# Kernel optimization log

Measured on AMD Instinct MI355X. Metric: run time of the kernel, lower is better.

Reference implementation:

```python
import jax, jax.numpy as jnp
import numpy as np
import math

B, S, N_UNITS, D_K = 8, 2048, 1024, 512


def setup_inputs() -> dict:
    key = jax.random.key(0)
    ks = jax.random.split(key, 8)
    scale = 1.0 / math.sqrt(N_UNITS)
    query = jax.random.normal(ks[0], (B, S, N_UNITS), dtype=jnp.float32)
    k_in = jax.random.normal(ks[1], (B, S, N_UNITS), dtype=jnp.float32)
    v_in = jax.random.normal(ks[2], (B, S, N_UNITS), dtype=jnp.float32)
    # custom multiplicative mask: causal lower-triangular, broadcast over batch
    mask = jnp.broadcast_to(jnp.tril(jnp.ones((S, S), dtype=jnp.float32)), (B, S, S))
    Wq = jax.random.normal(ks[3], (N_UNITS, D_K), dtype=jnp.float32) * scale
    Wk = jax.random.normal(ks[4], (N_UNITS, D_K), dtype=jnp.float32) * scale
    Wv = jax.random.normal(ks[5], (N_UNITS, D_K), dtype=jnp.float32) * scale
    bq = jnp.zeros((D_K,), dtype=jnp.float32)
    bk = jnp.zeros((D_K,), dtype=jnp.float32)
    bv = jnp.zeros((D_K,), dtype=jnp.float32)
    return {"query": query, "key": k_in, "value": v_in, "mask": mask,
            "Wq": Wq, "bq": bq, "Wk": Wk, "bk": bk, "Wv": Wv, "bv": bv}


def reference(query, key, value, mask, Wq, bq, Wk, bk, Wv, bv):
    d_k = Wq.shape[-1]
    Q = jnp.einsum('bsn,nd->bsd', query, Wq) + bq  # [B,S,Dk]
    K = jnp.einsum('bsn,nd->bsd', key, Wk) + bk
    V = jnp.einsum('bsn,nd->bsd', value, Wv) + bv
    # scores [B,S,S]
    x_hat = jnp.einsum('bqd,bkd->bqk', Q, K) / jnp.sqrt(jnp.float32(d_k))
    # custom multiplicative mask: x*mask - 1e9*(1-mask)
    x_hat_masked = x_hat * mask - 1e9 * (1.0 - mask)
    attn = jax.nn.softmax(x_hat_masked, axis=-1)
    # dropout = 0.0 (eval mode) -> identity
    out = jnp.einsum('bqk,bkd->bqd', attn, V)
    return out
```

## Files before the change

kernel.cpp:

```cpp
#include <hip/hip_runtime.h>

typedef __bf16 bf16_t;
typedef __attribute__((ext_vector_type(4))) __bf16 bf16x4;
typedef __attribute__((ext_vector_type(8))) __bf16 bf16x8;
typedef __attribute__((ext_vector_type(4))) float f32x4;

#define B_    8
#define S_    2048
#define NU    1024
#define DK    512
#define MROWS (B_ * S_)
#define PBATCH (128 * 128 * 136)

#define WAITVM(N) asm volatile("s_waitcnt vmcnt(" #N ")" ::: "memory")
#define WAITLG    asm volatile("s_waitcnt lgkmcnt(0)" ::: "memory")
#define BAR       __builtin_amdgcn_s_barrier()

__device__ __forceinline__ f32x4 mfma16(bf16x8 a, bf16x8 b, f32x4 c) {
  return __builtin_amdgcn_mfma_f32_16x16x32_bf16(a, b, c, 0, 0, 0);
}

__device__ __forceinline__ void async_load16(const void* g, void* l) {
  __builtin_amdgcn_global_load_lds(
      (const __attribute__((address_space(1))) unsigned int*)g,
      (__attribute__((address_space(3))) unsigned int*)l, 16, 0, 0);
}

__global__ __launch_bounds__(256) void transpose_w_kernel(
    const float* __restrict__ Wq, const float* __restrict__ Wk,
    const float* __restrict__ Wv, bf16_t* __restrict__ Wt) {
  const float* W = (blockIdx.z == 0) ? Wq : (blockIdx.z == 1) ? Wk : Wv;
  bf16_t* Wo = Wt + (size_t)blockIdx.z * DK * NU;
  __shared__ float tile[32][33];
  const int t = threadIdx.x;
  const int r = t >> 5, c = t & 31;
  const int kbase = blockIdx.y * 32, nbase = blockIdx.x * 32;
#pragma unroll
  for (int i = 0; i < 4; ++i)
    tile[r + i * 8][c] = W[(size_t)(kbase + r + i * 8) * DK + nbase + c];
  __syncthreads();
#pragma unroll
  for (int i = 0; i < 4; ++i)
    Wo[(size_t)(nbase + r + i * 8) * NU + kbase + c] = (bf16_t)tile[c][r + i * 8];
}

__global__ __launch_bounds__(256) void qkv_gemm_kernel(
    const float* __restrict__ q_in, const float* __restrict__ k_in,
    const float* __restrict__ v_in, const bf16_t* __restrict__ Wt,
    const float* __restrict__ bq, const float* __restrict__ bk,
    const float* __restrict__ bv, bf16_t* __restrict__ Qo,
    bf16_t* __restrict__ Ko, bf16_t* __restrict__ Vt) {
  const int z = blockIdx.y;
  const float* X = (z == 0) ? q_in : (z == 1) ? k_in : v_in;
  const bf16_t* Wz = Wt + (size_t)z * DK * NU;
  const float* bias = (z == 0) ? bq : (z == 1) ? bk : bv;

  __shared__ __align__(16) unsigned char smem[81920];
  float* A0 = (float*)smem;
  bf16_t* B0 = (bf16_t*)(smem + 8192);
  float* A1 = (float*)(smem + 40960);
  bf16_t* B1 = (bf16_t*)(smem + 49152);

  const int tid = threadIdx.x;
  const int wave = tid >> 6, lane = tid & 63;
  const int l16 = lane & 15, quad = lane >> 4;
  const int m0 = blockIdx.x * 64;
  const int ar = tid >> 3, ac = tid & 7;
  const int asrc = (ac ^ (ar & 7)) << 2;
  const int br = tid >> 2, bc = tid & 3;
  const int bsrc = (bc ^ (br & 3)) << 3;
  const int sw = l16 & 7;

  f32x4 acc[4][8] = {};

#define QKV_STAGE(An, Bn, K0)                                                 \
  { _Pragma("unroll") for (int j = 0; j < 2; ++j)                             \
      async_load16(X + (size_t)(m0 + j * 32 + ar) * NU + (K0) + asrc,         \
                   &(An)[(j * 32 + ar) * 32 + (ac << 2)]);                    \
    _Pragma("unroll") for (int j = 0; j < 8; ++j)                             \
      async_load16(Wz + (size_t)(j * 64 + br) * NU + (K0) + bsrc,             \
                   &(Bn)[(j * 64 + br) * 32 + (bc << 3)]); }

#define QKV_COMPUTE(Ac, Bc)                                                   \
  { bf16x8 af[4], bfr[8];                                                     \
    _Pragma("unroll") for (int i = 0; i < 4; ++i) {                           \
      const int row = i * 16 + l16;                                           \
      const f32x4 x0 = *(const f32x4*)&(Ac)[row * 32 + ((quad * 2) ^ sw) * 4];\
      const f32x4 x1 =                                                        \
          *(const f32x4*)&(Ac)[row * 32 + (((quad * 2) | 1) ^ sw) * 4];       \
      bf16x8 t;                                                               \
      _Pragma("unroll") for (int j = 0; j < 4; ++j) {                         \
        t[j] = (bf16_t)x0[j]; t[j + 4] = (bf16_t)x1[j]; }                     \
      af[i] = t; }                                                            \
    _Pragma("unroll") for (int j = 0; j < 8; ++j) {                           \
      const int row = wave * 128 + j * 16 + l16;                              \
      bfr[j] = *(const bf16x8*)&(Bc)[row * 32 + ((quad ^ (l16 & 3)) << 3)]; } \
    _Pragma("unroll") for (int i = 0; i < 4; ++i)                             \
      _Pragma("unroll") for (int j = 0; j < 8; ++j)                           \
        acc[i][j] = mfma16(af[i], bfr[j], acc[i][j]); }

  QKV_STAGE(A0, B0, 0)
  for (int ks = 0; ks < 32; ks += 2) {
    QKV_STAGE(A1, B1, (ks + 1) * 32)
    WAITVM(10); BAR;
    QKV_COMPUTE(A0, B0)
    WAITLG; BAR;
    if (ks + 2 < 32) { QKV_STAGE(A0, B0, (ks + 2) * 32) WAITVM(10); }
    else { WAITVM(0); }
    BAR;
    QKV_COMPUTE(A1, B1)
    WAITLG; BAR;
  }

  if (z != 2) {
    bf16_t* Out = (z == 0) ? Qo : Ko;
#pragma unroll
    for (int j = 0; j < 8; ++j) {
      const int cn = wave * 128 + j * 16 + l16;
      const float bz = bias[cn];
#pragma unroll
      for (int i = 0; i < 4; ++i) {
        const int rm = m0 + i * 16 + quad * 4;
#pragma unroll
        for (int r = 0; r < 4; ++r)
          Out[(size_t)(rm + r) * DK + cn] = (bf16_t)(acc[i][j][r] + bz);
      }
    }
  } else {
    bf16_t* Ts = (bf16_t*)smem;
#pragma unroll
    for (int j = 0; j < 8; ++j) {
      const int cn = wave * 128 + j * 16 + l16;
      const float bz = bias[cn];
#pragma unroll
      for (int i = 0; i < 4; ++i) {
        const int rs = i * 16 + quad * 4;
        bf16x4 t;
#pragma unroll
        for (int r = 0; r < 4; ++r) t[r] = (bf16_t)(acc[i][j][r] + bz);
        *(bf16x4*)&Ts[cn * 68 + rs] = t;
      }
    }
    WAITLG; BAR;
    const int bb = m0 >> 11, s0 = m0 & 2047;
#pragma unroll
    for (int rr = 0; rr < 2; ++rr) {
      const int row = rr * 256 + tid;
      bf16_t* dst = Vt + ((size_t)bb * DK + row) * S_ + s0;
      const bf16_t* src = &Ts[row * 68];
#pragma unroll
      for (int k = 0; k < 8; ++k)
        *(bf16x8*)(dst + k * 8) = *(const bf16x8*)(src + k * 8);
    }
  }
#undef QKV_STAGE
#undef QKV_COMPUTE
}

__global__ __launch_bounds__(256) void zerol_kernel(float* __restrict__ L) {
  ((f32x4*)L)[blockIdx.x * 256 + threadIdx.x] = f32x4{0.f, 0.f, 0.f, 0.f};
}

__global__ __launch_bounds__(256) void qk_p_kernel(
    const bf16_t* __restrict__ Q, const bf16_t* __restrict__ K,
    bf16_t* __restrict__ P, float* __restrict__ L) {
  const int bx = blockIdx.x;
  const int b = bx & 7;
  const int t = bx >> 3;
  int mt = 0;
  while (((mt + 1) * (mt + 2)) / 2 <= t) ++mt;
  const int nt = t - (mt * (mt + 1)) / 2;
  const int klen = (mt + 1) * 128;

  __shared__ __align__(16) bf16_t As[2][128 * 32];
  __shared__ __align__(16) bf16_t Bs[2][128 * 32];

  const int tid = threadIdx.x;
  const int wave = tid >> 6, lane = tid & 63;
  const int l16 = lane & 15, quad = lane >> 4;
  const int wm = (wave >> 1) * 64, wn = (wave & 1) * 64;
  const int br = tid >> 2, bc = tid & 3;
  const int bsrc = (bc ^ ((br >> 1) & 3)) << 3;
  const int sw2 = (l16 >> 1) & 3;

  const bf16_t* Ag = Q + (size_t)(b * S_ + mt * 128) * DK;
  const bf16_t* Bg = K + (size_t)(b * S_ + nt * 128) * DK;

  f32x4 acc[4][4] = {};

#define P1_STAGE(BUF, K0)                                                     \
  { _Pragma("unroll") for (int j = 0; j < 2; ++j)                             \
      async_load16(Ag + (size_t)(j * 64 + br) * DK + (K0) + bsrc,             \
                   &As[BUF][(j * 64 + br) * 32 + (bc << 3)]);                 \
    _Pragma("unroll") for (int j = 0; j < 2; ++j)                             \
      async_load16(Bg + (size_t)(j * 64 + br) * DK + (K0) + bsrc,             \
                   &Bs[BUF][(j * 64 + br) * 32 + (bc << 3)]); }

#define P1_COMPUTE(BUF)                                                       \
  { bf16x8 af[4], bfr[4];                                                     \
    _Pragma("unroll") for (int i = 0; i < 4; ++i)                             \
      af[i] = *(const bf16x8*)                                                \
          &As[BUF][(wm + i * 16 + l16) * 32 + ((quad ^ sw2) << 3)];           \
    _Pragma("unroll") for (int j = 0; j < 4; ++j)                             \
      bfr[j] = *(const bf16x8*)                                               \
          &Bs[BUF][(wn + j * 16 + l16) * 32 + ((quad ^ sw2) << 3)];           \
    _Pragma("unroll") for (int i = 0; i < 4; ++i)                             \
      _Pragma("unroll") for (int j = 0; j < 4; ++j)                           \
        acc[i][j] = mfma16(af[i], bfr[j], acc[i][j]); }

  P1_STAGE(0, 0)
  for (int ks = 0; ks < 16; ks += 2) {
    P1_STAGE(1, (ks + 1) * 32)
    WAITVM(4); BAR;
    P1_COMPUTE(0)
    WAITLG; BAR;
    if (ks + 2 < 16) { P1_STAGE(0, (ks + 2) * 32) WAITVM(4); }
    else { WAITVM(0); }
    BAR;
    P1_COMPUTE(1)
    WAITLG; BAR;
  }

  const float scale = 0.04419417382415922f;
  bf16_t* Pt = P + (size_t)b * PBATCH + (size_t)8192 * mt * (mt + 1);
  float* Lb = L + b * S_ + mt * 128;
#pragma unroll
  for (int i = 0; i < 4; ++i) {
#pragma unroll
    for (int r = 0; r < 4; ++r) {
      const int lrow = wm + i * 16 + quad * 4 + r;
      const int srow = mt * 128 + lrow;
      float rsum = 0.f;
#pragma unroll
      for (int j = 0; j < 4; ++j) {
        const int scol = nt * 128 + wn + j * 16 + l16;
        const float p =
            (scol > srow) ? 0.f : __expf(acc[i][j][r] * scale - 10.0f);
        rsum += p;
        Pt[(size_t)lrow * klen + scol] = (bf16_t)p;
      }
#pragma unroll
      for (int off = 8; off >= 1; off >>= 1)
        rsum += __shfl_xor(rsum, off, 64);
      if (l16 == 0) atomicAdd(&Lb[lrow], rsum);
    }
  }
#undef P1_STAGE
#undef P1_COMPUTE
}

__global__ __launch_bounds__(256) void pv_kernel(
    const bf16_t* __restrict__ P, const bf16_t* __restrict__ Vt,
    const float* __restrict__ L, float* __restrict__ Out) {
  const int bx = blockIdx.x;
  const int b = bx & 7;
  const int u = bx >> 3;
  const int mt = 15 - (u >> 2);
  const int d0 = (u & 3) * 128;
  const int klen = (mt + 1) * 128;
  const int NS = (mt + 1) * 4;

  __shared__ __align__(16) bf16_t As[2][128 * 32];
  __shared__ __align__(16) bf16_t Bs[2][128 * 32];

  const int tid = threadIdx.x;
  const int wave = tid >> 6, lane = tid & 63;
  const int l16 = lane & 15, quad = lane >> 4;
  const int wm = (wave >> 1) * 64, wn = (wave & 1) * 64;
  const int br = tid >> 2, bc = tid & 3;
  const int bsrc = (bc ^ ((br >> 1) & 3)) << 3;
  const int sw2 = (l16 >> 1) & 3;

  const bf16_t* Ag = P + (size_t)b * PBATCH + (size_t)8192 * mt * (mt + 1);
  const bf16_t* Bg = Vt + ((size_t)b * DK + d0) * S_;

  f32x4 acc[4][4] = {};

#define P2_STAGE(BUF, K0)                                                     \
  { _Pragma("unroll") for (int j = 0; j < 2; ++j)                             \
      async_load16(Ag + (size_t)(j * 64 + br) * klen + (K0) + bsrc,           \
                   &As[BUF][(j * 64 + br) * 32 + (bc << 3)]);                 \
    _Pragma("unroll") for (int j = 0; j < 2; ++j)                             \
      async_load16(Bg + (size_t)(j * 64 + br) * S_ + (K0) + bsrc,             \
                   &Bs[BUF][(j * 64 + br) * 32 + (bc << 3)]); }

#define P2_COMPUTE(BUF)                                                       \
  { bf16x8 af[4], bfr[4];                                                     \
    _Pragma("unroll") for (int i = 0; i < 4; ++i)                             \
      af[i] = *(const bf16x8*)                                                \
          &As[BUF][(wm + i * 16 + l16) * 32 + ((quad ^ sw2) << 3)];           \
    _Pragma("unroll") for (int j = 0; j < 4; ++j)                             \
      bfr[j] = *(const bf16x8*)                                               \
          &Bs[BUF][(wn + j * 16 + l16) * 32 + ((quad ^ sw2) << 3)];           \
    _Pragma("unroll") for (int i = 0; i < 4; ++i)                             \
      _Pragma("unroll") for (int j = 0; j < 4; ++j)                           \
        acc[i][j] = mfma16(af[i], bfr[j], acc[i][j]); }

  P2_STAGE(0, 0)
  for (int ks = 0; ks < NS; ks += 2) {
    P2_STAGE(1, (ks + 1) * 32)
    WAITVM(4); BAR;
    P2_COMPUTE(0)
    WAITLG; BAR;
    if (ks + 2 < NS) { P2_STAGE(0, (ks + 2) * 32) WAITVM(4); }
    else { WAITVM(0); }
    BAR;
    P2_COMPUTE(1)
    WAITLG; BAR;
  }

  const int m0 = b * S_ + mt * 128;
#pragma unroll
  for (int i = 0; i < 4; ++i) {
#pragma unroll
    for (int r = 0; r < 4; ++r) {
      const int grow = m0 + wm + i * 16 + quad * 4 + r;
      const float inv = 1.0f / L[grow];
      float* orow = Out + (size_t)grow * DK + d0;
#pragma unroll
      for (int j = 0; j < 4; ++j)
        orow[wn + j * 16 + l16] = acc[i][j][r] * inv;
    }
  }
#undef P2_STAGE
#undef P2_COMPUTE
}

extern "C" void kernel_launch(void* const* d_in, const int* in_sizes, int n_in,
                              void* d_out, int out_size, void* d_ws, size_t ws_size,
                              hipStream_t stream) {
  const float* query = (const float*)d_in[0];
  const float* key_i = (const float*)d_in[1];
  const float* value = (const float*)d_in[2];
  const float* Wq = (const float*)d_in[4];
  const float* bq = (const float*)d_in[5];
  const float* Wk = (const float*)d_in[6];
  const float* bk = (const float*)d_in[7];
  const float* Wv = (const float*)d_in[8];
  const float* bv = (const float*)d_in[9];
  float* out = (float*)d_out;

  bf16_t* Wt = (bf16_t*)d_ws;
  bf16_t* Qw = Wt + (size_t)3 * DK * NU;
  bf16_t* Kw = Qw + (size_t)MROWS * DK;
  bf16_t* Vw = Kw + (size_t)MROWS * DK;
  bf16_t* Pw = Vw + (size_t)MROWS * DK;
  float* Lw = (float*)(Pw + (size_t)B_ * PBATCH);

  transpose_w_kernel<<<dim3(16, 32, 3), 256, 0, stream>>>(Wq, Wk, Wv, Wt);
  zerol_kernel<<<16, 256, 0, stream>>>(Lw);
  qkv_gemm_kernel<<<dim3(256, 3), 256, 0, stream>>>(
      query, key_i, value, Wt, bq, bk, bv, Qw, Kw, Vw);
  qk_p_kernel<<<1088, 256, 0, stream>>>(Qw, Kw, Pw, Lw);
  pv_kernel<<<512, 256, 0, stream>>>(Pw, Vw, Lw, out);
}
```

Before: 468.5 us.

## Pre-convert inputs to bf16, retile QKV GEMM, add triple-buffered pipelines

The fused fp32-input QKV GEMM is replaced by a separate fp32-to-bf16 conversion pass into the P workspace, followed by three 128x128-tile bf16 GEMMs that reuse a shared staging helper. All three GEMM-style kernels now use a three-stage LDS ring with one barrier pair per k-step instead of double buffering, a new swizzled layout, and launch bounds requesting 3 blocks per CU. The aim is to halve the A-tile LDS traffic, drop in-loop conversion, and hide more load latency. The cost is an extra read and write pass over the inputs plus six more kernel launches.

Result: faster. 458.9 us (-2.1%).

```diff
diff --git a/kernel.cpp b/kernel.cpp
--- a/kernel.cpp
+++ b/kernel.cpp
@@ -24,6 +24,32 @@
   __builtin_amdgcn_global_load_lds(
       (const __attribute__((address_space(1))) unsigned int*)g,
       (__attribute__((address_space(3))) unsigned int*)l, 16, 0, 0);
+}
+
+__device__ __forceinline__ bf16x8 cvt8(f32x4 x0, f32x4 x1) {
+  bf16x8 r;
+#pragma unroll
+  for (int j = 0; j < 4; ++j) { r[j] = (bf16_t)x0[j]; r[j + 4] = (bf16_t)x1[j]; }
+  return r;
+}
+
+__device__ __forceinline__ void stage_tile(const bf16_t* __restrict__ src,
+                                           int rstride, bf16_t* dst, int k0,
+                                           int tid) {
+#pragma unroll
+  for (int j = 0; j < 2; ++j) {
+    const int g = j * 256 + tid;
+    const int ln = g >> 3, c = g & 7;
+    const int cs = c ^ (ln & 7);
+    const int srow = 2 * ln + (cs >> 2);
+    async_load16(src + (size_t)srow * rstride + k0 + (cs & 3) * 8, dst + g * 8);
+  }
+}
+
+__device__ __forceinline__ bf16x8 frag(const bf16_t* buf, int row, int q) {
+  const int ln = row >> 1;
+  const int cp = (((row & 1) << 2) | q) ^ (ln & 7);
+  return *(const bf16x8*)(buf + ln * 64 + cp * 8);
 }
 
 __global__ __launch_bounds__(256) void transpose_w_kernel(
@@ -44,83 +70,75 @@
     Wo[(size_t)(nbase + r + i * 8) * NU + kbase + c] = (bf16_t)tile[c][r + i * 8];
 }
 
-__global__ __launch_bounds__(256) void qkv_gemm_kernel(
-    const float* __restrict__ q_in, const float* __restrict__ k_in,
-    const float* __restrict__ v_in, const bf16_t* __restrict__ Wt,
-    const float* __restrict__ bq, const float* __restrict__ bk,
-    const float* __restrict__ bv, bf16_t* __restrict__ Qo,
-    bf16_t* __restrict__ Ko, bf16_t* __restrict__ Vt) {
-  const int z = blockIdx.y;
-  const float* X = (z == 0) ? q_in : (z == 1) ? k_in : v_in;
-  const bf16_t* Wz = Wt + (size_t)z * DK * NU;
-  const float* bias = (z == 0) ? bq : (z == 1) ? bk : bv;
-
-  __shared__ __align__(16) unsigned char smem[81920];
-  float* A0 = (float*)smem;
-  bf16_t* B0 = (bf16_t*)(smem + 8192);
-  float* A1 = (float*)(smem + 40960);
-  bf16_t* B1 = (bf16_t*)(smem + 49152);
-
+__global__ __launch_bounds__(256) void cvt_kernel(const float* __restrict__ src,
+                                                  bf16_t* __restrict__ dst) {
+  const size_t t0 = (size_t)blockIdx.x * 256 + threadIdx.x;
+#pragma unroll
+  for (int it = 0; it < 8; ++it) {
+    const size_t i = t0 + (size_t)it * 262144;
+    const f32x4 x0 = ((const f32x4*)src)[2 * i];
+    const f32x4 x1 = ((const f32x4*)src)[2 * i + 1];
+    ((bf16x8*)dst)[i] = cvt8(x0, x1);
+  }
+}
+
+__global__ __launch_bounds__(256, 3) void xw_gemm_kernel(
+    const bf16_t* __restrict__ Xz, const bf16_t* __restrict__ Wz,
+    const float* __restrict__ bias, bf16_t* __restrict__ Out, const int vmode) {
+  const int bx = blockIdx.x;
+  const int m0 = (bx & 127) * 128;
+  const int n0 = (bx >> 7) * 128;
   const int tid = threadIdx.x;
   const int wave = tid >> 6, lane = tid & 63;
   const int l16 = lane & 15, quad = lane >> 4;
-  const int m0 = blockIdx.x * 64;
-  const int ar = tid >> 3, ac = tid & 7;
-  const int asrc = (ac ^ (ar & 7)) << 2;
-  const int br = tid >> 2, bc = tid & 3;
-  const int bsrc = (bc ^ (br & 3)) << 3;
-  const int sw = l16 & 7;
-
-  f32x4 acc[4][8] = {};
-
-#define QKV_STAGE(An, Bn, K0)                                                 \
-  { _Pragma("unroll") for (int j = 0; j < 2; ++j)                             \
-      async_load16(X + (size_t)(m0 + j * 32 + ar) * NU + (K0) + asrc,         \
-                   &(An)[(j * 32 + ar) * 32 + (ac << 2)]);                    \
-    _Pragma("unroll") for (int j = 0; j < 8; ++j)                             \
-      async_load16(Wz + (size_t)(j * 64 + br) * NU + (K0) + bsrc,             \
-                   &(Bn)[(j * 64 + br) * 32 + (bc << 3)]); }
-
-#define QKV_COMPUTE(Ac, Bc)                                                   \
-  { bf16x8 af[4], bfr[8];                                                     \
-    _Pragma("unroll") for (int i = 0; i < 4; ++i) {                           \
-      const int row = i * 16 + l16;                                           \
-      const f32x4 x0 = *(const f32x4*)&(Ac)[row * 32 + ((quad * 2) ^ sw) * 4];\
-      const f32x4 x1 =                                                        \
-          *(const f32x4*)&(Ac)[row * 32 + (((quad * 2) | 1) ^ sw) * 4];       \
-      bf16x8 t;                                                               \
-      _Pragma("unroll") for (int j = 0; j < 4; ++j) {                         \
-        t[j] = (bf16_t)x0[j]; t[j + 4] = (bf16_t)x1[j]; }                     \
-      af[i] = t; }                                                            \
-    _Pragma("unroll") for (int j = 0; j < 8; ++j) {                           \
-      const int row = wave * 128 + j * 16 + l16;                              \
-      bfr[j] = *(const bf16x8*)&(Bc)[row * 32 + ((quad ^ (l16 & 3)) << 3)]; } \
-    _Pragma("unroll") for (int i = 0; i < 4; ++i)                             \
-      _Pragma("unroll") for (int j = 0; j < 8; ++j)                           \
+  const int wm = (wave >> 1) * 64, wn = (wave & 1) * 64;
+
+  __shared__ __align__(16) unsigned char smem[49152];
+  bf16_t* a0 = (bf16_t*)smem;
+  bf16_t* a1 = (bf16_t*)(smem + 8192);
+  bf16_t* a2 = (bf16_t*)(smem + 16384);
+  bf16_t* b0 = (bf16_t*)(smem + 24576);
+  bf16_t* b1 = (bf16_t*)(smem + 32768);
+  bf16_t* b2 = (bf16_t*)(smem + 40960);
+
+  const bf16_t* Ag = Xz + (size_t)m0 * NU;
+  const bf16_t* Bg = Wz + (size_t)n0 * NU;
+
+  f32x4 acc[4][4] = {};
+
+#define XW_STAGE(Ad, Bd, K0) \
+  { stage_tile(Ag, NU, Ad, K0, tid); stage_tile(Bg, NU, Bd, K0, tid); }
+#define XW_COMP(Ac, Bc)                                                       \
+  { bf16x8 af[4], bfr[4];                                                     \
+    _Pragma("unroll") for (int i = 0; i < 4; ++i)                             \
+      af[i] = frag(Ac, wm + i * 16 + l16, quad);                              \
+    _Pragma("unroll") for (int j = 0; j < 4; ++j)                             \
+      bfr[j] = frag(Bc, wn + j * 16 + l16, quad);                             \
+    _Pragma("unroll") for (int i = 0; i < 4; ++i)                             \
+      _Pragma("unroll") for (int j = 0; j < 4; ++j)                           \
         acc[i][j] = mfma16(af[i], bfr[j], acc[i][j]); }
 
-  QKV_STAGE(A0, B0, 0)
-  for (int ks = 0; ks < 32; ks += 2) {
-    QKV_STAGE(A1, B1, (ks + 1) * 32)
-    WAITVM(10); BAR;
-    QKV_COMPUTE(A0, B0)
+  XW_STAGE(a0, b0, 0)
+  XW_STAGE(a1, b1, 32)
+  const int NS = 32;
+  for (int ks = 0; ks < NS; ++ks) {
+    if (ks + 1 < NS) { WAITVM(4); } else { WAITVM(0); }
+    BAR;
+    if (ks + 2 < NS) XW_STAGE(a2, b2, (ks + 2) * 32)
+    XW_COMP(a0, b0)
     WAITLG; BAR;
-    if (ks + 2 < 32) { QKV_STAGE(A0, B0, (ks + 2) * 32) WAITVM(10); }
-    else { WAITVM(0); }
-    BAR;
-    QKV_COMPUTE(A1, B1)
-    WAITLG; BAR;
-  }
-
-  if (z != 2) {
-    bf16_t* Out = (z == 0) ? Qo : Ko;
-#pragma unroll
-    for (int j = 0; j < 8; ++j) {
-      const int cn = wave * 128 + j * 16 + l16;
+    bf16_t* t = a0; a0 = a1; a1 = a2; a2 = t;
+    t = b0; b0 = b1; b1 = b2; b2 = t;
+  }
+
+  if (vmode == 0) {
+#pragma unroll
+    for (int j = 0; j < 4; ++j) {
+      const int cn = n0 + wn + j * 16 + l16;
       const float bz = bias[cn];
 #pragma unroll
       for (int i = 0; i < 4; ++i) {
-        const int rm = m0 + i * 16 + quad * 4;
+        const int rm = m0 + wm + i * 16 + quad * 4;
 #pragma unroll
         for (int r = 0; r < 4; ++r)
           Out[(size_t)(rm + r) * DK + cn] = (bf16_t)(acc[i][j][r] + bz);
@@ -129,39 +147,36 @@
   } else {
     bf16_t* Ts = (bf16_t*)smem;
 #pragma unroll
-    for (int j = 0; j < 8; ++j) {
-      const int cn = wave * 128 + j * 16 + l16;
-      const float bz = bias[cn];
+    for (int j = 0; j < 4; ++j) {
+      const int cnl = wn + j * 16 + l16;
+      const float bz = bias[n0 + cnl];
 #pragma unroll
       for (int i = 0; i < 4; ++i) {
-        const int rs = i * 16 + quad * 4;
+        const int rs = wm + i * 16 + quad * 4;
         bf16x4 t;
 #pragma unroll
         for (int r = 0; r < 4; ++r) t[r] = (bf16_t)(acc[i][j][r] + bz);
-        *(bf16x4*)&Ts[cn * 68 + rs] = t;
+        *(bf16x4*)&Ts[cnl * 136 + rs] = t;
       }
     }
     WAITLG; BAR;
-    const int bb = m0 >> 11, s0 = m0 & 2047;
-#pragma unroll
-    for (int rr = 0; rr < 2; ++rr) {
-      const int row = rr * 256 + tid;
-      bf16_t* dst = Vt + ((size_t)bb * DK + row) * S_ + s0;
-      const bf16_t* src = &Ts[row * 68];
-#pragma unroll
-      for (int k = 0; k < 8; ++k)
-        *(bf16x8*)(dst + k * 8) = *(const bf16x8*)(src + k * 8);
-    }
-  }
-#undef QKV_STAGE
-#undef QKV_COMPUTE
+    const int bb = m0 >> 11, sl = m0 & 2047;
+    const int row = tid >> 1, half = tid & 1;
+    bf16_t* dst = Out + ((size_t)bb * DK + n0 + row) * S_ + sl + half * 64;
+    const bf16_t* sp = &Ts[row * 136 + half * 64];
+#pragma unroll
+    for (int k = 0; k < 8; ++k)
+      *(bf16x8*)(dst + k * 8) = *(const bf16x8*)(sp + k * 8);
+  }
+#undef XW_STAGE
+#undef XW_COMP
 }
 
 __global__ __launch_bounds__(256) void zerol_kernel(float* __restrict__ L) {
   ((f32x4*)L)[blockIdx.x * 256 + threadIdx.x] = f32x4{0.f, 0.f, 0.f, 0.f};
 }
 
-__global__ __launch_bounds__(256) void qk_p_kernel(
+__global__ __launch_bounds__(256, 3) void qk_p_kernel(
     const bf16_t* __restrict__ Q, const bf16_t* __restrict__ K,
     bf16_t* __restrict__ P, float* __restrict__ L) {
   const int bx = blockIdx.x;
@@ -172,53 +187,47 @@
   const int nt = t - (mt * (mt + 1)) / 2;
   const int klen = (mt + 1) * 128;
 
-  __shared__ __align__(16) bf16_t As[2][128 * 32];
-  __shared__ __align__(16) bf16_t Bs[2][128 * 32];
-
   const int tid = threadIdx.x;
   const int wave = tid >> 6, lane = tid & 63;
   const int l16 = lane & 15, quad = lane >> 4;
   const int wm = (wave >> 1) * 64, wn = (wave & 1) * 64;
-  const int br = tid >> 2, bc = tid & 3;
-  const int bsrc = (bc ^ ((br >> 1) & 3)) << 3;
-  const int sw2 = (l16 >> 1) & 3;
+
+  __shared__ __align__(16) unsigned char smem[49152];
+  bf16_t* a0 = (bf16_t*)smem;
+  bf16_t* a1 = (bf16_t*)(smem + 8192);
+  bf16_t* a2 = (bf16_t*)(smem + 16384);
+  bf16_t* b0 = (bf16_t*)(smem + 24576);
+  bf16_t* b1 = (bf16_t*)(smem + 32768);
+  bf16_t* b2 = (bf16_t*)(smem + 40960);
 
   const bf16_t* Ag = Q + (size_t)(b * S_ + mt * 128) * DK;
   const bf16_t* Bg = K + (size_t)(b * S_ + nt * 128) * DK;
 
   f32x4 acc[4][4] = {};
 
-#define P1_STAGE(BUF, K0)                                                     \
-  { _Pragma("unroll") for (int j = 0; j < 2; ++j)                             \
-      async_load16(Ag + (size_t)(j * 64 + br) * DK + (K0) + bsrc,             \
-                   &As[BUF][(j * 64 + br) * 32 + (bc << 3)]);                 \
-    _Pragma("unroll") for (int j = 0; j < 2; ++j)                             \
-      async_load16(Bg + (size_t)(j * 64 + br) * DK + (K0) + bsrc,             \
-                   &Bs[BUF][(j * 64 + br) * 32 + (bc << 3)]); }
-
-#define P1_COMPUTE(BUF)                                                       \
+#define P1_STAGE(Ad, Bd, K0) \
+  { stage_tile(Ag, DK, Ad, K0, tid); stage_tile(Bg, DK, Bd, K0, tid); }
+#define P1_COMP(Ac, Bc)                                                       \
   { bf16x8 af[4], bfr[4];                                                     \
     _Pragma("unroll") for (int i = 0; i < 4; ++i)                             \
-      af[i] = *(const bf16x8*)                                                \
-          &As[BUF][(wm + i * 16 + l16) * 32 + ((quad ^ sw2) << 3)];           \
+      af[i] = frag(Ac, wm + i * 16 + l16, quad);                              \
     _Pragma("unroll") for (int j = 0; j < 4; ++j)                             \
-      bfr[j] = *(const bf16x8*)                                               \
-          &Bs[BUF][(wn + j * 16 + l16) * 32 + ((quad ^ sw2) << 3)];           \
+      bfr[j] = frag(Bc, wn + j * 16 + l16, quad);                             \
     _Pragma("unroll") for (int i = 0; i < 4; ++i)                             \
       _Pragma("unroll") for (int j = 0; j < 4; ++j)                           \
         acc[i][j] = mfma16(af[i], bfr[j], acc[i][j]); }
 
-  P1_STAGE(0, 0)
-  for (int ks = 0; ks < 16; ks += 2) {
-    P1_STAGE(1, (ks + 1) * 32)
-    WAITVM(4); BAR;
-    P1_COMPUTE(0)
+  P1_STAGE(a0, b0, 0)
+  P1_STAGE(a1, b1, 32)
+  const int NS = 16;
+  for (int ks = 0; ks < NS; ++ks) {
+    if (ks + 1 < NS) { WAITVM(4); } else { WAITVM(0); }
+    BAR;
+    if (ks + 2 < NS) P1_STAGE(a2, b2, (ks + 2) * 32)
+    P1_COMP(a0, b0)
     WAITLG; BAR;
-    if (ks + 2 < 16) { P1_STAGE(0, (ks + 2) * 32) WAITVM(4); }
-    else { WAITVM(0); }
-    BAR;
-    P1_COMPUTE(1)
-    WAITLG; BAR;
+    bf16_t* tp = a0; a0 = a1; a1 = a2; a2 = tp;
+    tp = b0; b0 = b1; b1 = b2; b2 = tp;
   }
 
   const float scale = 0.04419417382415922f;
@@ -246,10 +255,10 @@
     }
   }
 #undef P1_STAGE
-#undef P1_COMPUTE
-}
-
-__global__ __launch_bounds__(256) void pv_kernel(
+#undef P1_COMP
+}
+
+__global__ __launch_bounds__(256, 3) void pv_kernel(
     const bf16_t* __restrict__ P, const bf16_t* __restrict__ Vt,
     const float* __restrict__ L, float* __restrict__ Out) {
   const int bx = blockIdx.x;
@@ -260,53 +269,46 @@
   const int klen = (mt + 1) * 128;
   const int NS = (mt + 1) * 4;
 
-  __shared__ __align__(16) bf16_t As[2][128 * 32];
-  __shared__ __align__(16) bf16_t Bs[2][128 * 32];
-
   const int tid = threadIdx.x;
   const int wave = tid >> 6, lane = tid & 63;
   const int l16 = lane & 15, quad = lane >> 4;
   const int wm = (wave >> 1) * 64, wn = (wave & 1) * 64;
-  const int br = tid >> 2, bc = tid & 3;
-  const int bsrc = (bc ^ ((br >> 1) & 3)) << 3;
-  const int sw2 = (l16 >> 1) & 3;
+
+  __shared__ __align__(16) unsigned char smem[49152];
+  bf16_t* a0 = (bf16_t*)smem;
+  bf16_t* a1 = (bf16_t*)(smem + 8192);
+  bf16_t* a2 = (bf16_t*)(smem + 16384);
+  bf16_t* b0 = (bf16_t*)(smem + 24576);
+  bf16_t* b1 = (bf16_t*)(smem + 32768);
+  bf16_t* b2 = (bf16_t*)(smem + 40960);
 
   const bf16_t* Ag = P + (size_t)b * PBATCH + (size_t)8192 * mt * (mt + 1);
   const bf16_t* Bg = Vt + ((size_t)b * DK + d0) * S_;
 
   f32x4 acc[4][4] = {};
 
-#define P2_STAGE(BUF, K0)                                                     \
-  { _Pragma("unroll") for (int j = 0; j < 2; ++j)                             \
-      async_load16(Ag + (size_t)(j * 64 + br) * klen + (K0) + bsrc,           \
-                   &As[BUF][(j * 64 + br) * 32 + (bc << 3)]);                 \
-    _Pragma("unroll") for (int j = 0; j < 2; ++j)                             \
-      async_load16(Bg + (size_t)(j * 64 + br) * S_ + (K0) + bsrc,             \
-                   &Bs[BUF][(j * 64 + br) * 32 + (bc << 3)]); }
-
-#define P2_COMPUTE(BUF)                                                       \
+#define P2_STAGE(Ad, Bd, K0) \
+  { stage_tile(Ag, klen, Ad, K0, tid); stage_tile(Bg, S_, Bd, K0, tid); }
+#define P2_COMP(Ac, Bc)                                                       \
   { bf16x8 af[4], bfr[4];                                                     \
     _Pragma("unroll") for (int i = 0; i < 4; ++i)                             \
-      af[i] = *(const bf16x8*)                                                \
-          &As[BUF][(wm + i * 16 + l16) * 32 + ((quad ^ sw2) << 3)];           \
+      af[i] = frag(Ac, wm + i * 16 + l16, quad);                              \
     _Pragma("unroll") for (int j = 0; j < 4; ++j)                             \
-      bfr[j] = *(const bf16x8*)                                               \
-          &Bs[BUF][(wn + j * 16 + l16) * 32 + ((quad ^ sw2) << 3)];           \
+      bfr[j] = frag(Bc, wn + j * 16 + l16, quad);                             \
     _Pragma("unroll") for (int i = 0; i < 4; ++i)                             \
       _Pragma("unroll") for (int j = 0; j < 4; ++j)                           \
         acc[i][j] = mfma16(af[i], bfr[j], acc[i][j]); }
 
-  P2_STAGE(0, 0)
-  for (int ks = 0; ks < NS; ks += 2) {
-    P2_STAGE(1, (ks + 1) * 32)
-    WAITVM(4); BAR;
-    P2_COMPUTE(0)
+  P2_STAGE(a0, b0, 0)
+  P2_STAGE(a1, b1, 32)
+  for (int ks = 0; ks < NS; ++ks) {
+    if (ks + 1 < NS) { WAITVM(4); } else { WAITVM(0); }
+    BAR;
+    if (ks + 2 < NS) P2_STAGE(a2, b2, (ks + 2) * 32)
+    P2_COMP(a0, b0)
     WAITLG; BAR;
-    if (ks + 2 < NS) { P2_STAGE(0, (ks + 2) * 32) WAITVM(4); }
-    else { WAITVM(0); }
-    BAR;
-    P2_COMPUTE(1)
-    WAITLG; BAR;
+    bf16_t* tp = a0; a0 = a1; a1 = a2; a2 = tp;
+    tp = b0; b0 = b1; b1 = b2; b2 = tp;
   }
 
   const int m0 = b * S_ + mt * 128;
@@ -323,7 +325,7 @@
     }
   }
 #undef P2_STAGE
-#undef P2_COMPUTE
+#undef P2_COMP
 }
 
 extern "C" void kernel_launch(void* const* d_in, const int* in_sizes, int n_in,
@@ -345,12 +347,19 @@
   bf16_t* Kw = Qw + (size_t)MROWS * DK;
   bf16_t* Vw = Kw + (size_t)MROWS * DK;
   bf16_t* Pw = Vw + (size_t)MROWS * DK;
+  bf16_t* Xz = Pw;
   float* Lw = (float*)(Pw + (size_t)B_ * PBATCH);
 
   transpose_w_kernel<<<dim3(16, 32, 3), 256, 0, stream>>>(Wq, Wk, Wv, Wt);
   zerol_kernel<<<16, 256, 0, stream>>>(Lw);
-  qkv_gemm_kernel<<<dim3(256, 3), 256, 0, stream>>>(
-      query, key_i, value, Wt, bq, bk, bv, Qw, Kw, Vw);
+
+  cvt_kernel<<<1024, 256, 0, stream>>>(query, Xz);
+  xw_gemm_kernel<<<512, 256, 0, stream>>>(Xz, Wt, bq, Qw, 0);
+  cvt_kernel<<<1024, 256, 0, stream>>>(key_i, Xz);
+  xw_gemm_kernel<<<512, 256, 0, stream>>>(Xz, Wt + (size_t)DK * NU, bk, Kw, 0);
+  cvt_kernel<<<1024, 256, 0, stream>>>(value, Xz);
+  xw_gemm_kernel<<<512, 256, 0, stream>>>(Xz, Wt + (size_t)2 * DK * NU, bv, Vw, 1);
+
   qk_p_kernel<<<1088, 256, 0, stream>>>(Qw, Kw, Pw, Lw);
   pv_kernel<<<512, 256, 0, stream>>>(Pw, Vw, Lw, out);
 }
```
